# Kernel optimization log

Measured on AMD Instinct MI355X. Metric: run time of the kernel, lower is better.

## Reference

```python
import jax, jax.numpy as jnp
import numpy as np

N_NODES = 50000
N_EDGES = 800000
IN_FEATS = 256
H_FEATS = 256
NUM_CLASSES = 16
NUM_GRAPHS = 64


def _glorot(key, shape):
    lim = float(np.sqrt(6.0 / (shape[0] + shape[1])))
    return jax.random.uniform(key, shape, jnp.float32, -lim, lim)


def setup_inputs() -> dict:
    key = jax.random.key(0)
    ks = jax.random.split(key, 12)
    x = jax.random.normal(ks[0], (N_NODES, IN_FEATS), jnp.float32)
    edge_index = jax.random.randint(ks[1], (2, N_EDGES), 0, N_NODES, jnp.int64)
    batch_vec = jnp.sort(jax.random.randint(ks[2], (N_NODES,), 0, NUM_GRAPHS, jnp.int64))
    W1 = _glorot(ks[3], (IN_FEATS, H_FEATS)); b1 = jnp.zeros((H_FEATS,), jnp.float32)
    W2 = _glorot(ks[4], (H_FEATS, H_FEATS)); b2 = jnp.zeros((H_FEATS,), jnp.float32)
    W3 = _glorot(ks[5], (H_FEATS, H_FEATS)); b3 = jnp.zeros((H_FEATS,), jnp.float32)
    W4 = _glorot(ks[6], (H_FEATS, NUM_CLASSES)); b4 = jnp.zeros((NUM_CLASSES,), jnp.float32)
    return {"x": x, "edge_index": edge_index, "batch_vec": batch_vec,
            "W1": W1, "b1": b1, "W2": W2, "b2": b2,
            "W3": W3, "b3": b3, "W4": W4, "b4": b4}


def gcn_conv(x, W, b, src, dst, deg_inv_sqrt):
    # PyG GCNConv: out = D^{-1/2} (A + I) D^{-1/2} (x W) + b
    h = x @ W  # [N, F_out]
    norm = deg_inv_sqrt[src] * deg_inv_sqrt[dst]  # [E+N]
    msgs = h[src] * norm[:, None]  # gather + scale
    agg = jax.ops.segment_sum(msgs, dst, num_segments=x.shape[0])
    return agg + b


def reference(x, edge_index, batch_vec, W1, b1, W2, b2, W3, b3, W4, b4):
    n = x.shape[0]
    # add self-loops once (shared across layers)
    loops = jnp.arange(n, dtype=edge_index.dtype)
    src = jnp.concatenate([edge_index[0], loops])
    dst = jnp.concatenate([edge_index[1], loops])
    deg = jax.ops.segment_sum(jnp.ones_like(dst, dtype=x.dtype), dst, num_segments=n)
    deg_inv_sqrt = jnp.where(deg > 0, jax.lax.rsqrt(deg), 0.0)

    h = gcn_conv(x, W1, b1, src, dst, deg_inv_sqrt)
    h_copy = jax.nn.relu(h)
    # dropout is identity in eval mode (training=False)
    h = gcn_conv(h_copy, W2, b2, src, dst, deg_inv_sqrt)
    h_copy = jax.nn.relu(jax.nn.relu(h) + h_copy)
    h = gcn_conv(h_copy, W3, b3, src, dst, deg_inv_sqrt)
    h = jax.nn.relu(jax.nn.relu(h) + h_copy)
    h = gcn_conv(h, W4, b4, src, dst, deg_inv_sqrt)

    # global_mean_pool over batch vector
    sums = jax.ops.segment_sum(h, batch_vec, num_segments=NUM_GRAPHS)
    counts = jax.ops.segment_sum(jnp.ones((n,), h.dtype), batch_vec, num_segments=NUM_GRAPHS)
    return sums / jnp.maximum(counts, 1.0)[:, None]
```

## Files before the change

### kernel.cpp

```cpp
#include <hip/hip_runtime.h>
#include <hip/hip_bf16.h>

#define N_NODES 50000
#define N_EDGES 800000
#define F 256
#define NGRAPH 64
#define NCLS 16
#define NBLK_N 196

typedef short short8 __attribute__((ext_vector_type(8)));
typedef float f32x4 __attribute__((ext_vector_type(4)));

__device__ __forceinline__ float bf2f(ushort u) {
    unsigned v = ((unsigned)u) << 16;
    return __uint_as_float(v);
}
__device__ __forceinline__ ushort f2bf(float f) {
    __hip_bfloat16 b = __float2bfloat16(f);
    return *reinterpret_cast<ushort*>(&b);
}
__device__ __forceinline__ float bflo(uint u) { return __uint_as_float(u << 16); }
__device__ __forceinline__ float bfhi(uint u) { return __uint_as_float(u & 0xffff0000u); }


__global__ __launch_bounds__(256) void k_zero_int(int* __restrict__ p, int n) {
    int i = blockIdx.x * 256 + threadIdx.x;
    if (i < n) p[i] = 0;
}

__global__ __launch_bounds__(256) void k_count(const int* __restrict__ dst,
                                               int* __restrict__ ecnt) {
    int e = blockIdx.x * 256 + threadIdx.x;
    if (e < N_EDGES) atomicAdd(&ecnt[dst[e]], 1);
}

__global__ __launch_bounds__(256) void k_scan_block(const int* __restrict__ ecnt,
                                                    int* __restrict__ rowptr,
                                                    int* __restrict__ blkSum,
                                                    float* __restrict__ dinv) {
    __shared__ int sh[256];
    int i = blockIdx.x * 256 + threadIdx.x;
    int v = (i < N_NODES) ? ecnt[i] : 0;
    sh[threadIdx.x] = v;
    __syncthreads();
#pragma unroll
    for (int off = 1; off < 256; off <<= 1) {
        int t = (threadIdx.x >= off) ? sh[threadIdx.x - off] : 0;
        __syncthreads();
        sh[threadIdx.x] += t;
        __syncthreads();
    }
    if (i < N_NODES) {
        rowptr[i] = sh[threadIdx.x] - v;
        dinv[i] = rsqrtf((float)(v + 1));
    }
    if (threadIdx.x == 255) blkSum[blockIdx.x] = sh[255];
}

__global__ __launch_bounds__(256) void k_scan_tops(int* __restrict__ blkSum,
                                                   int* __restrict__ blkOff) {
    __shared__ int sh[256];
    int v = (threadIdx.x < NBLK_N) ? blkSum[threadIdx.x] : 0;
    sh[threadIdx.x] = v;
    __syncthreads();
#pragma unroll
    for (int off = 1; off < 256; off <<= 1) {
        int t = (threadIdx.x >= off) ? sh[threadIdx.x - off] : 0;
        __syncthreads();
        sh[threadIdx.x] += t;
        __syncthreads();
    }
    if (threadIdx.x < NBLK_N) blkOff[threadIdx.x] = sh[threadIdx.x] - v;
}

__global__ __launch_bounds__(256) void k_scan_add(int* __restrict__ rowptr,
                                                  const int* __restrict__ blkOff,
                                                  int* __restrict__ cursor) {
    int i = blockIdx.x * 256 + threadIdx.x;
    if (i < N_NODES) {
        int r = rowptr[i] + blkOff[blockIdx.x];
        rowptr[i] = r;
        cursor[i] = r;
    }
    if (i == 0) rowptr[N_NODES] = N_EDGES;
}

__global__ __launch_bounds__(256) void k_fill_csr(const int* __restrict__ src,
                                                  const int* __restrict__ dst,
                                                  int* __restrict__ cursor,
                                                  ushort* __restrict__ csr16) {
    int e = blockIdx.x * 256 + threadIdx.x;
    if (e >= N_EDGES) return;
    int s = src[e];
    int d = dst[e];
    int p = atomicAdd(&cursor[d], 1);
    csr16[p] = (ushort)s;
}


__global__ __launch_bounds__(256) void k_cast_bf16(const float* __restrict__ in,
                                                   ushort* __restrict__ out,
                                                   int n8) {
    int i = blockIdx.x * 256 + threadIdx.x;
    if (i >= n8) return;
    const float4* ip = (const float4*)(in + (size_t)i * 8);
    float4 a = ip[0], b = ip[1];
    short8 v;
    v[0] = (short)f2bf(a.x); v[1] = (short)f2bf(a.y);
    v[2] = (short)f2bf(a.z); v[3] = (short)f2bf(a.w);
    v[4] = (short)f2bf(b.x); v[5] = (short)f2bf(b.y);
    v[6] = (short)f2bf(b.z); v[7] = (short)f2bf(b.w);
    *(short8*)(out + (size_t)i * 8) = v;
}

__global__ __launch_bounds__(256) void k_wpack(const float* __restrict__ W,
                                               ushort* __restrict__ Wp) {
    int idx = blockIdx.x * 256 + threadIdx.x;
    if (idx >= 16 * 8 * 64) return;
    int lane = idx & 63;
    int ks = (idx >> 6) & 7;
    int ctg = idx >> 9;
    int kbase = ks * 32 + (lane >> 4) * 8;
    int col = ctg * 16 + (lane & 15);
    short8 v;
#pragma unroll
    for (int e = 0; e < 8; ++e)
        v[e] = (short)f2bf(W[(size_t)(kbase + e) * 256 + col]);
    *(short8*)(Wp + (size_t)idx * 8) = v;
}


__global__ __launch_bounds__(256, 2) void k_mfma256(const ushort* __restrict__ Ab,
                                                    const ushort* __restrict__ Wp,
                                                    const float* __restrict__ dinv,
                                                    ushort* __restrict__ C) {
    const int t = threadIdx.x;
    const int wv = t >> 6;
    const int l = t & 63;
    const int m0 = blockIdx.x * 64;
    const int colbase = wv * 64;
    const int lrow = l & 15;
    const int lk = (l >> 4) * 8;

    short8 wf[4][8];
    const short8* wp = (const short8*)Wp;
#pragma unroll
    for (int ct = 0; ct < 4; ++ct)
#pragma unroll
        for (int ks = 0; ks < 8; ++ks)
            wf[ct][ks] = wp[(size_t)(((wv * 4 + ct) * 8 + ks) * 64) + l];

#pragma unroll
    for (int msub = 0; msub < 4; ++msub) {
        int arow = m0 + msub * 16 + lrow;
        if (arow >= N_NODES) arow = N_NODES - 1;
        const ushort* ap = Ab + (size_t)arow * F + lk;
        short8 af[8];
#pragma unroll
        for (int ks = 0; ks < 8; ++ks)
            af[ks] = *(const short8*)(ap + ks * 32);

        f32x4 acc[4];
#pragma unroll
        for (int ct = 0; ct < 4; ++ct) acc[ct] = (f32x4){0.f, 0.f, 0.f, 0.f};
#pragma unroll
        for (int ks = 0; ks < 8; ++ks)
#pragma unroll
            for (int ct = 0; ct < 4; ++ct)
                acc[ct] = __builtin_amdgcn_mfma_f32_16x16x32_bf16(af[ks], wf[ct][ks], acc[ct], 0, 0, 0);

        int orow0 = m0 + msub * 16 + (l >> 4) * 4;
        float dv[4];
#pragma unroll
        for (int r = 0; r < 4; ++r)
            dv[r] = (orow0 + r < N_NODES) ? dinv[orow0 + r] : 0.f;
#pragma unroll
        for (int ct = 0; ct < 4; ++ct) {
            int ocol = colbase + ct * 16 + (l & 15);
#pragma unroll
            for (int r = 0; r < 4; ++r) {
                int orow = orow0 + r;
                if (orow < N_NODES)
                    C[(size_t)orow * F + ocol] = f2bf(acc[ct][r] * dv[r]);
            }
        }
    }
}


template <int MODE>
__global__ __launch_bounds__(256) void k_gather256(const ushort* __restrict__ H,
                                                   const float* __restrict__ bias,
                                                   const float* __restrict__ dinv,
                                                   const int* __restrict__ rowptr,
                                                   const ushort* __restrict__ csr16,
                                                   const ushort* __restrict__ hc,
                                                   ushort* __restrict__ OUT) {
    int gid = blockIdx.x * 256 + threadIdx.x;
    int n = gid >> 6;
    int lane = gid & 63;
    if (n >= N_NODES) return;
    const int slot = lane >> 5;
    const int c = (lane & 31) * 8;

    float acc[8];
#pragma unroll
    for (int j = 0; j < 8; ++j) acc[j] = 0.f;

    int i = rowptr[n] + slot;
    const int end = rowptr[n + 1];
    for (; i + 6 < end; i += 8) {
        int s0 = csr16[i], s1 = csr16[i + 2], s2 = csr16[i + 4], s3 = csr16[i + 6];
        short8 v0 = *(const short8*)(H + (size_t)s0 * F + c);
        short8 v1 = *(const short8*)(H + (size_t)s1 * F + c);
        short8 v2 = *(const short8*)(H + (size_t)s2 * F + c);
        short8 v3 = *(const short8*)(H + (size_t)s3 * F + c);
#pragma unroll
        for (int j = 0; j < 8; ++j)
            acc[j] += (bf2f((ushort)v0[j]) + bf2f((ushort)v1[j])) +
                      (bf2f((ushort)v2[j]) + bf2f((ushort)v3[j]));
    }
    for (; i < end; i += 2) {
        int s0 = csr16[i];
        short8 v0 = *(const short8*)(H + (size_t)s0 * F + c);
#pragma unroll
        for (int j = 0; j < 8; ++j) acc[j] += bf2f((ushort)v0[j]);
    }

#pragma unroll
    for (int j = 0; j < 8; ++j) acc[j] += __shfl_xor(acc[j], 32);

    if (slot == 0) {
        const short8 h = *(const short8*)(H + (size_t)n * F + c);
        const float4 b0 = *(const float4*)(bias + c);
        const float4 b1 = *(const float4*)(bias + c + 4);
        float bb[8] = {b0.x, b0.y, b0.z, b0.w, b1.x, b1.y, b1.z, b1.w};
        float di = dinv[n];
        float s[8];
#pragma unroll
        for (int j = 0; j < 8; ++j)
            s[j] = bb[j] + di * (acc[j] + bf2f((ushort)h[j]));

        short8 ov;
        if (MODE == 1) {
#pragma unroll
            for (int j = 0; j < 8; ++j)
                ov[j] = (short)f2bf(fmaxf(s[j], 0.f));
        } else {
            const short8 hv = *(const short8*)(hc + (size_t)n * F + c);
#pragma unroll
            for (int j = 0; j < 8; ++j)
                ov[j] = (short)f2bf(fmaxf(fmaxf(s[j], 0.f) + bf2f((ushort)hv[j]), 0.f));
        }
        *(short8*)(OUT + (size_t)n * F + c) = ov;
    }
}


__global__ __launch_bounds__(256) void k_gemm16(const ushort* __restrict__ A,
                                                const float* __restrict__ W4,
                                                const float* __restrict__ dinv,
                                                ushort* __restrict__ C) {
    __shared__ float Ws[256][16];
    const int t = threadIdx.x;
    {
        const float4* wp = (const float4*)(W4 + (size_t)t * 16);
        float4 a = wp[0], b = wp[1], c = wp[2], d = wp[3];
        float4* sp = (float4*)&Ws[t][0];
        sp[0] = a; sp[1] = b; sp[2] = c; sp[3] = d;
    }
    __syncthreads();
    int row = blockIdx.x * 256 + t;
    if (row >= N_NODES) return;
    const short8* ap = (const short8*)(A + (size_t)row * F);
    float acc[16];
#pragma unroll
    for (int c = 0; c < 16; ++c) acc[c] = 0.f;
    for (int k8 = 0; k8 < 32; ++k8) {
        short8 a8 = ap[k8];
#pragma unroll
        for (int j = 0; j < 8; ++j) {
            float av = bf2f((ushort)a8[j]);
            const float4* wr = (const float4*)&Ws[k8 * 8 + j][0];
            float4 w0 = wr[0], w1 = wr[1], w2 = wr[2], w3 = wr[3];
            acc[0]  += av * w0.x; acc[1]  += av * w0.y;
            acc[2]  += av * w0.z; acc[3]  += av * w0.w;
            acc[4]  += av * w1.x; acc[5]  += av * w1.y;
            acc[6]  += av * w1.z; acc[7]  += av * w1.w;
            acc[8]  += av * w2.x; acc[9]  += av * w2.y;
            acc[10] += av * w2.z; acc[11] += av * w2.w;
            acc[12] += av * w3.x; acc[13] += av * w3.y;
            acc[14] += av * w3.z; acc[15] += av * w3.w;
        }
    }
    float dv = dinv[row];
    short8 o0, o1;
#pragma unroll
    for (int c = 0; c < 8; ++c) o0[c] = (short)f2bf(acc[c] * dv);
#pragma unroll
    for (int c = 0; c < 8; ++c) o1[c] = (short)f2bf(acc[8 + c] * dv);
    short8* op = (short8*)(C + (size_t)row * 16);
    op[0] = o0; op[1] = o1;
}


__global__ __launch_bounds__(256) void k_g16pool(const ushort* __restrict__ G16,
                                                 const float* __restrict__ bias,
                                                 const float* __restrict__ dinv,
                                                 const int* __restrict__ rowptr,
                                                 const ushort* __restrict__ csr16,
                                                 const int* __restrict__ batch,
                                                 float* __restrict__ pool,
                                                 float* __restrict__ cnt) {
    __shared__ float ps[NGRAPH][NCLS];
    __shared__ float pc[NGRAPH];
    for (int i = threadIdx.x; i < NGRAPH * NCLS; i += 256) ((float*)ps)[i] = 0.f;
    if (threadIdx.x < NGRAPH) pc[threadIdx.x] = 0.f;
    __syncthreads();

    int gid = blockIdx.x * 256 + threadIdx.x;
    int n = gid >> 2;
    int q = (gid & 3) * 4;
    if (n < N_NODES) {
        float ax = 0.f, ay = 0.f, az = 0.f, aw = 0.f;
        const int end = rowptr[n + 1];
        for (int i = rowptr[n]; i < end; ++i) {
            int s0 = csr16[i];
            const uint2 u = *(const uint2*)(G16 + (size_t)s0 * 16 + q);
            ax += bflo(u.x); ay += bfhi(u.x);
            az += bflo(u.y); aw += bfhi(u.y);
        }
        const uint2 hu = *(const uint2*)(G16 + (size_t)n * 16 + q);
        const float4 b = *(const float4*)(bias + q);
        float di = dinv[n];
        int g = batch[n];
        atomicAdd(&ps[g][q + 0], b.x + di * (ax + bflo(hu.x)));
        atomicAdd(&ps[g][q + 1], b.y + di * (ay + bfhi(hu.x)));
        atomicAdd(&ps[g][q + 2], b.z + di * (az + bflo(hu.y)));
        atomicAdd(&ps[g][q + 3], b.w + di * (aw + bfhi(hu.y)));
        if ((gid & 3) == 0) atomicAdd(&pc[g], 1.f);
    }
    __syncthreads();

    for (int i = threadIdx.x; i < NGRAPH * NCLS; i += 256) {
        float v = ((float*)ps)[i];
        if (v != 0.f) unsafeAtomicAdd(&pool[i], v);
    }
    if (threadIdx.x < NGRAPH) {
        float v = pc[threadIdx.x];
        if (v > 0.f) unsafeAtomicAdd(&cnt[threadIdx.x], v);
    }
}

__global__ __launch_bounds__(256) void k_pool_zero(float* __restrict__ pool,
                                                   float* __restrict__ cnt) {
    int i = blockIdx.x * 256 + threadIdx.x;
    if (i < NGRAPH * NCLS) pool[i] = 0.f;
    if (i < NGRAPH) cnt[i] = 0.f;
}

__global__ __launch_bounds__(256) void k_final(const float* __restrict__ pool,
                                               const float* __restrict__ cnt,
                                               float* __restrict__ out) {
    int i = blockIdx.x * 256 + threadIdx.x;
    if (i < NGRAPH * NCLS) out[i] = pool[i] / fmaxf(cnt[i >> 4], 1.f);
}


extern "C" void kernel_launch(void* const* d_in, const int* in_sizes, int n_in,
                              void* d_out, int out_size, void* d_ws, size_t ws_size,
                              hipStream_t stream) {
    const float* x   = (const float*)d_in[0];
    const int*   ei  = (const int*)d_in[1];
    const int*   bvec= (const int*)d_in[2];
    const float* W1  = (const float*)d_in[3];
    const float* b1  = (const float*)d_in[4];
    const float* W2  = (const float*)d_in[5];
    const float* b2  = (const float*)d_in[6];
    const float* W3  = (const float*)d_in[7];
    const float* b3  = (const float*)d_in[8];
    const float* W4  = (const float*)d_in[9];
    const float* b4  = (const float*)d_in[10];
    float* out = (float*)d_out;

    const int* src = ei;
    const int* dst = ei + N_EDGES;

    const size_t NF = (size_t)N_NODES * F;
    float* ws = (float*)d_ws;
    ushort* XA = (ushort*)ws;
    ushort* XB = XA + NF;
    ushort* Hg = XB + NF;
    ushort* G16 = (ushort*)(ws + 3 * NF / 2);
    float*  aux = ws + 3 * NF / 2 + 400000;
    int*    ecnt   = (int*)aux;
    float*  dinv   = aux + N_NODES;
    int*    rowptr = (int*)(aux + 2 * N_NODES);
    int*    cursor = (int*)(aux + 3 * N_NODES + 64);
    int*    blkSum = (int*)(aux + 4 * N_NODES + 64);
    int*    blkOff = blkSum + 256;
    ushort* csr16  = (ushort*)(blkOff + 256);
    float*  pool   = (float*)(csr16 + N_EDGES);
    float*  cnt    = pool + NGRAPH * NCLS;
    ushort* Wp1    = (ushort*)(cnt + NGRAPH);
    ushort* Wp2    = Wp1 + 65536;
    ushort* Wp3    = Wp2 + 65536;

    const int BN = NBLK_N;
    const int BE = (N_EDGES + 255) / 256;
    const int BM = (N_NODES + 63) / 64;
    const int BG = (N_NODES * 64 + 255) / 256;
    const int B4 = (N_NODES * 4 + 255) / 256;
    const int BC = (int)((NF / 8 + 255) / 256);

    k_zero_int<<<BN, 256, 0, stream>>>(ecnt, N_NODES);
    k_pool_zero<<<5, 256, 0, stream>>>(pool, cnt);
    k_count<<<BE, 256, 0, stream>>>(dst, ecnt);
    k_scan_block<<<BN, 256, 0, stream>>>(ecnt, rowptr, blkSum, dinv);
    k_scan_tops<<<1, 256, 0, stream>>>(blkSum, blkOff);
    k_scan_add<<<BN, 256, 0, stream>>>(rowptr, blkOff, cursor);
    k_fill_csr<<<BE, 256, 0, stream>>>(src, dst, cursor, csr16);

    k_cast_bf16<<<BC, 256, 0, stream>>>(x, XA, (int)(NF / 8));
    k_wpack<<<32, 256, 0, stream>>>(W1, Wp1);
    k_wpack<<<32, 256, 0, stream>>>(W2, Wp2);
    k_wpack<<<32, 256, 0, stream>>>(W3, Wp3);

    k_mfma256<<<BM, 256, 0, stream>>>(XA, Wp1, dinv, Hg);
    k_gather256<1><<<BG, 256, 0, stream>>>(Hg, b1, dinv, rowptr, csr16, nullptr, XB);

    k_mfma256<<<BM, 256, 0, stream>>>(XB, Wp2, dinv, Hg);
    k_gather256<2><<<BG, 256, 0, stream>>>(Hg, b2, dinv, rowptr, csr16, XB, XA);

    k_mfma256<<<BM, 256, 0, stream>>>(XA, Wp3, dinv, Hg);
    k_gather256<2><<<BG, 256, 0, stream>>>(Hg, b3, dinv, rowptr, csr16, XA, XB);

    k_gemm16<<<BN, 256, 0, stream>>>(XB, W4, dinv, G16);
    k_g16pool<<<B4, 256, 0, stream>>>(G16, b4, dinv, rowptr, csr16, bvec, pool, cnt);

    k_final<<<4, 256, 0, stream>>>(pool, cnt, out);
}
```

Before: 439.3 us.

## Fuse input cast into first GEMM, merge setup kernels, coalesce GEMM stores via LDS

Drops the standalone fp32-to-bf16 cast of x by converting in the first MFMA GEMM's A-operand load. Folds three weight-pack launches into one, merges the zero kernels, and replaces the separate top-level scan with a per-block reduction of the preceding block sums. GEMM output is staged through shared memory so each row is written with 16-byte vector stores instead of scattered 2-byte stores. The result is fewer launches and less global traffic, at the cost of extra LDS use and redundant reductions in the scan.

```diff
diff --git a/kernel.cpp b/kernel.cpp
--- a/kernel.cpp
+++ b/kernel.cpp
@@ -23,9 +23,13 @@
 __device__ __forceinline__ float bfhi(uint u) { return __uint_as_float(u & 0xffff0000u); }
 
 
-__global__ __launch_bounds__(256) void k_zero_int(int* __restrict__ p, int n) {
+__global__ __launch_bounds__(256) void k_init(int* __restrict__ ecnt,
+                                              float* __restrict__ pool,
+                                              float* __restrict__ cnt) {
     int i = blockIdx.x * 256 + threadIdx.x;
-    if (i < n) p[i] = 0;
+    if (i < N_NODES) ecnt[i] = 0;
+    if (i < NGRAPH * NCLS) pool[i] = 0.f;
+    if (i < NGRAPH) cnt[i] = 0.f;
 }
 
 __global__ __launch_bounds__(256) void k_count(const int* __restrict__ dst,
@@ -57,28 +61,22 @@
     if (threadIdx.x == 255) blkSum[blockIdx.x] = sh[255];
 }
 
-__global__ __launch_bounds__(256) void k_scan_tops(int* __restrict__ blkSum,
-                                                   int* __restrict__ blkOff) {
+__global__ __launch_bounds__(256) void k_scan_add(const int* __restrict__ blkSum,
+                                                  int* __restrict__ rowptr,
+                                                  int* __restrict__ cursor) {
     __shared__ int sh[256];
-    int v = (threadIdx.x < NBLK_N) ? blkSum[threadIdx.x] : 0;
-    sh[threadIdx.x] = v;
+    int t = threadIdx.x;
+    sh[t] = (t < NBLK_N && t < (int)blockIdx.x) ? blkSum[t] : 0;
     __syncthreads();
 #pragma unroll
-    for (int off = 1; off < 256; off <<= 1) {
-        int t = (threadIdx.x >= off) ? sh[threadIdx.x - off] : 0;
+    for (int off = 128; off > 0; off >>= 1) {
+        if (t < off) sh[t] += sh[t + off];
         __syncthreads();
-        sh[threadIdx.x] += t;
-        __syncthreads();
-    }
-    if (threadIdx.x < NBLK_N) blkOff[threadIdx.x] = sh[threadIdx.x] - v;
-}
-
-__global__ __launch_bounds__(256) void k_scan_add(int* __restrict__ rowptr,
-                                                  const int* __restrict__ blkOff,
-                                                  int* __restrict__ cursor) {
-    int i = blockIdx.x * 256 + threadIdx.x;
+    }
+    int base = sh[0];
+    int i = blockIdx.x * 256 + t;
     if (i < N_NODES) {
-        int r = rowptr[i] + blkOff[blockIdx.x];
+        int r = rowptr[i] + base;
         rowptr[i] = r;
         cursor[i] = r;
     }
@@ -98,25 +96,15 @@
 }
 
 
-__global__ __launch_bounds__(256) void k_cast_bf16(const float* __restrict__ in,
-                                                   ushort* __restrict__ out,
-                                                   int n8) {
-    int i = blockIdx.x * 256 + threadIdx.x;
-    if (i >= n8) return;
-    const float4* ip = (const float4*)(in + (size_t)i * 8);
-    float4 a = ip[0], b = ip[1];
-    short8 v;
-    v[0] = (short)f2bf(a.x); v[1] = (short)f2bf(a.y);
-    v[2] = (short)f2bf(a.z); v[3] = (short)f2bf(a.w);
-    v[4] = (short)f2bf(b.x); v[5] = (short)f2bf(b.y);
-    v[6] = (short)f2bf(b.z); v[7] = (short)f2bf(b.w);
-    *(short8*)(out + (size_t)i * 8) = v;
-}
-
-__global__ __launch_bounds__(256) void k_wpack(const float* __restrict__ W,
-                                               ushort* __restrict__ Wp) {
-    int idx = blockIdx.x * 256 + threadIdx.x;
-    if (idx >= 16 * 8 * 64) return;
+__global__ __launch_bounds__(256) void k_wpack3(const float* __restrict__ W1,
+                                                const float* __restrict__ W2,
+                                                const float* __restrict__ W3,
+                                                ushort* __restrict__ Wp) {
+    int gid = blockIdx.x * 256 + threadIdx.x;
+    int which = gid >> 13;
+    int idx = gid & 8191;
+    const float* W = (which == 0) ? W1 : (which == 1) ? W2 : W3;
+    ushort* o = Wp + (size_t)which * 65536;
     int lane = idx & 63;
     int ks = (idx >> 6) & 7;
     int ctg = idx >> 9;
@@ -126,14 +114,16 @@
 #pragma unroll
     for (int e = 0; e < 8; ++e)
         v[e] = (short)f2bf(W[(size_t)(kbase + e) * 256 + col]);
-    *(short8*)(Wp + (size_t)idx * 8) = v;
-}
-
-
-__global__ __launch_bounds__(256, 2) void k_mfma256(const ushort* __restrict__ Ab,
+    *(short8*)(o + (size_t)idx * 8) = v;
+}
+
+
+template <int F32IN>
+__global__ __launch_bounds__(256, 2) void k_mfma256(const void* __restrict__ Av,
                                                     const ushort* __restrict__ Wp,
                                                     const float* __restrict__ dinv,
                                                     ushort* __restrict__ C) {
+    __shared__ __align__(16) ushort cs[4][16 * 64];
     const int t = threadIdx.x;
     const int wv = t >> 6;
     const int l = t & 63;
@@ -154,11 +144,24 @@
     for (int msub = 0; msub < 4; ++msub) {
         int arow = m0 + msub * 16 + lrow;
         if (arow >= N_NODES) arow = N_NODES - 1;
-        const ushort* ap = Ab + (size_t)arow * F + lk;
         short8 af[8];
-#pragma unroll
-        for (int ks = 0; ks < 8; ++ks)
-            af[ks] = *(const short8*)(ap + ks * 32);
+        if (F32IN) {
+            const float* ap = (const float*)Av + (size_t)arow * F + lk;
+#pragma unroll
+            for (int ks = 0; ks < 8; ++ks) {
+                float4 a0 = *(const float4*)(ap + ks * 32);
+                float4 a1 = *(const float4*)(ap + ks * 32 + 4);
+                af[ks][0] = (short)f2bf(a0.x); af[ks][1] = (short)f2bf(a0.y);
+                af[ks][2] = (short)f2bf(a0.z); af[ks][3] = (short)f2bf(a0.w);
+                af[ks][4] = (short)f2bf(a1.x); af[ks][5] = (short)f2bf(a1.y);
+                af[ks][6] = (short)f2bf(a1.z); af[ks][7] = (short)f2bf(a1.w);
+            }
+        } else {
+            const ushort* ap = (const ushort*)Av + (size_t)arow * F + lk;
+#pragma unroll
+            for (int ks = 0; ks < 8; ++ks)
+                af[ks] = *(const short8*)(ap + ks * 32);
+        }
 
         f32x4 acc[4];
 #pragma unroll
@@ -174,15 +177,24 @@
 #pragma unroll
         for (int r = 0; r < 4; ++r)
             dv[r] = (orow0 + r < N_NODES) ? dinv[orow0 + r] : 0.f;
+
 #pragma unroll
         for (int ct = 0; ct < 4; ++ct) {
-            int ocol = colbase + ct * 16 + (l & 15);
+            int col = ct * 16 + (l & 15);
 #pragma unroll
             for (int r = 0; r < 4; ++r) {
-                int orow = orow0 + r;
-                if (orow < N_NODES)
-                    C[(size_t)orow * F + ocol] = f2bf(acc[ct][r] * dv[r]);
+                int row = (l >> 4) * 4 + r;
+                cs[wv][row * 64 + col] = f2bf(acc[ct][r] * dv[r]);
             }
+        }
+#pragma unroll
+        for (int h = 0; h < 2; ++h) {
+            int row = h * 8 + (l >> 3);
+            int coff = (l & 7) * 8;
+            short8 v = *(const short8*)&cs[wv][row * 64 + coff];
+            int orow = m0 + msub * 16 + row;
+            if (orow < N_NODES)
+                *(short8*)(C + (size_t)orow * F + colbase + coff) = v;
         }
     }
 }
@@ -350,13 +362,6 @@
         float v = pc[threadIdx.x];
         if (v > 0.f) unsafeAtomicAdd(&cnt[threadIdx.x], v);
     }
-}
-
-__global__ __launch_bounds__(256) void k_pool_zero(float* __restrict__ pool,
-                                                   float* __restrict__ cnt) {
-    int i = blockIdx.x * 256 + threadIdx.x;
-    if (i < NGRAPH * NCLS) pool[i] = 0.f;
-    if (i < NGRAPH) cnt[i] = 0.f;
 }
 
 __global__ __launch_bounds__(256) void k_final(const float* __restrict__ pool,
@@ -387,55 +392,45 @@
     const int* dst = ei + N_EDGES;
 
     const size_t NF = (size_t)N_NODES * F;
-    float* ws = (float*)d_ws;
-    ushort* XA = (ushort*)ws;
-    ushort* XB = XA + NF;
-    ushort* Hg = XB + NF;
-    ushort* G16 = (ushort*)(ws + 3 * NF / 2);
-    float*  aux = ws + 3 * NF / 2 + 400000;
+    ushort* P   = (ushort*)d_ws;
+    ushort* Q   = P + NF;
+    ushort* Hg  = Q + NF;
+    ushort* G16 = Hg + NF;
+    float*  aux = (float*)(G16 + (size_t)N_NODES * 16 + 64);
     int*    ecnt   = (int*)aux;
     float*  dinv   = aux + N_NODES;
     int*    rowptr = (int*)(aux + 2 * N_NODES);
     int*    cursor = (int*)(aux + 3 * N_NODES + 64);
     int*    blkSum = (int*)(aux + 4 * N_NODES + 64);
-    int*    blkOff = blkSum + 256;
-    ushort* csr16  = (ushort*)(blkOff + 256);
+    ushort* csr16  = (ushort*)(blkSum + 256);
     float*  pool   = (float*)(csr16 + N_EDGES);
     float*  cnt    = pool + NGRAPH * NCLS;
-    ushort* Wp1    = (ushort*)(cnt + NGRAPH);
-    ushort* Wp2    = Wp1 + 65536;
-    ushort* Wp3    = Wp2 + 65536;
+    ushort* Wp     = (ushort*)(cnt + NGRAPH);
 
     const int BN = NBLK_N;
     const int BE = (N_EDGES + 255) / 256;
     const int BM = (N_NODES + 63) / 64;
     const int BG = (N_NODES * 64 + 255) / 256;
     const int B4 = (N_NODES * 4 + 255) / 256;
-    const int BC = (int)((NF / 8 + 255) / 256);
-
-    k_zero_int<<<BN, 256, 0, stream>>>(ecnt, N_NODES);
-    k_pool_zero<<<5, 256, 0, stream>>>(pool, cnt);
+
+    k_init<<<BN, 256, 0, stream>>>(ecnt, pool, cnt);
     k_count<<<BE, 256, 0, stream>>>(dst, ecnt);
     k_scan_block<<<BN, 256, 0, stream>>>(ecnt, rowptr, blkSum, dinv);
-    k_scan_tops<<<1, 256, 0, stream>>>(blkSum, blkOff);
-    k_scan_add<<<BN, 256, 0, stream>>>(rowptr, blkOff, cursor);
+    k_scan_add<<<BN, 256, 0, stream>>>(blkSum, rowptr, cursor);
     k_fill_csr<<<BE, 256, 0, stream>>>(src, dst, cursor, csr16);
 
-    k_cast_bf16<<<BC, 256, 0, stream>>>(x, XA, (int)(NF / 8));
-    k_wpack<<<32, 256, 0, stream>>>(W1, Wp1);
-    k_wpack<<<32, 256, 0, stream>>>(W2, Wp2);
-    k_wpack<<<32, 256, 0, stream>>>(W3, Wp3);
-
-    k_mfma256<<<BM, 256, 0, stream>>>(XA, Wp1, dinv, Hg);
-    k_gather256<1><<<BG, 256, 0, stream>>>(Hg, b1, dinv, rowptr, csr16, nullptr, XB);
-
-    k_mfma256<<<BM, 256, 0, stream>>>(XB, Wp2, dinv, Hg);
-    k_gather256<2><<<BG, 256, 0, stream>>>(Hg, b2, dinv, rowptr, csr16, XB, XA);
-
-    k_mfma256<<<BM, 256, 0, stream>>>(XA, Wp3, dinv, Hg);
-    k_gather256<2><<<BG, 256, 0, stream>>>(Hg, b3, dinv, rowptr, csr16, XA, XB);
-
-    k_gemm16<<<BN, 256, 0, stream>>>(XB, W4, dinv, G16);
+    k_wpack3<<<96, 256, 0, stream>>>(W1, W2, W3, Wp);
+
+    k_mfma256<1><<<BM, 256, 0, stream>>>(x, Wp, dinv, Hg);
+    k_gather256<1><<<BG, 256, 0, stream>>>(Hg, b1, dinv, rowptr, csr16, nullptr, P);
+
+    k_mfma256<0><<<BM, 256, 0, stream>>>(P, Wp + 65536, dinv, Hg);
+    k_gather256<2><<<BG, 256, 0, stream>>>(Hg, b2, dinv, rowptr, csr16, P, Q);
+
+    k_mfma256<0><<<BM, 256, 0, stream>>>(Q, Wp + 131072, dinv, Hg);
+    k_gather256<2><<<BG, 256, 0, stream>>>(Hg, b3, dinv, rowptr, csr16, Q, P);
+
+    k_gemm16<<<BN, 256, 0, stream>>>(P, W4, dinv, G16);
     k_g16pool<<<B4, 256, 0, stream>>>(G16, b4, dinv, rowptr, csr16, bvec, pool, cnt);
 
     k_final<<<4, 256, 0, stream>>>(pool, cnt, out);
```

After: 402.1 us. 1.09x faster.
